# Kernel optimization log

Hardware: AMD Instinct MI355X
Metric: run time of the kernel (lower is better)

## Reference

```python
import jax, jax.numpy as jnp
import numpy as np

K = 4          # torus_dim (circles)
M = 6          # n_modes
GRID = 12      # grid_size for Laplacian eigenvalues
T = 2.0        # uniformity temperature
SPREAD_W = 1.0
B = 8192       # batch size


def _karmonic_weights():
    # lambda_n = 2 - 2 cos(2 pi n / N), n = 1..M; w = (lam - lam1)/(lam_max - lam1)
    n = np.arange(1, M + 1)
    lam = 2.0 - 2.0 * np.cos(2.0 * np.pi * n / GRID)
    w = (lam - lam[0]) / (lam.max() - lam[0])
    return jnp.asarray(w, dtype=jnp.float32)


def setup_inputs() -> dict:
    key = jax.random.key(0)
    k1, k2 = jax.random.split(key)
    angles = jax.random.normal(k1, (B, K), dtype=jnp.float32)
    fourier_embed = jax.random.normal(k2, (B, 2 * K * M), dtype=jnp.float32)
    return {"angles": angles, "fourier_embed": fourier_embed}


def reference(angles, fourier_embed):
    Bn = fourier_embed.shape[0]
    w = _karmonic_weights()
    # group by mode: (B, M, 2K)
    x = fourier_embed.reshape(Bn, M, 2 * K)
    eye = jnp.eye(Bn, dtype=bool)
    log_Bm1 = jnp.log(jnp.float32(Bn - 1))

    total_unif = jnp.float32(0.0)
    mode_unifs = []
    for n in range(M):  # fixed small structural loop over modes
        xn = x[:, n, :]                                   # (B, 2K)
        sq = jnp.sum(xn * xn, axis=1)                     # (B,)
        d2 = sq[:, None] + sq[None, :] - 2.0 * (xn @ xn.T)
        d2 = jnp.maximum(d2, 0.0)                         # cdist(...)**2, clamped >= 0
        neg = jnp.where(eye, -jnp.inf, -T * d2)           # exclude diagonal like masked_select
        unif_n = jnp.mean(jax.nn.logsumexp(neg, axis=1)) - log_Bm1
        mode_unifs.append(unif_n)
        total_unif = total_unif + w[n] * unif_n

    # circular decorrelation (spread) across circle pairs, vectorized over pairs
    mu = jnp.arctan2(jnp.mean(jnp.sin(angles), axis=0),
                     jnp.mean(jnp.cos(angles), axis=0))   # (K,) circular means
    s = jnp.sin(angles - mu[None, :])                     # (B, K)
    cov = (s.T @ s) / jnp.float32(Bn)                     # (K, K) = mean(s_i * s_j)
    var = jnp.diagonal(cov)                               # mean(s_i^2)
    den = jnp.sqrt(var[:, None] * var[None, :] + 1e-8)
    corr2 = (cov / den) ** 2
    iu = np.triu_indices(K, 1)                            # upper-triangle pairs i<j
    spread = jnp.mean(corr2[iu])

    total = total_unif + jnp.float32(SPREAD_W) * spread
    return total_unif, spread, total, jnp.stack(mode_unifs)
```

## Files before the change

kernel.cpp:

```cpp
#include <hip/hip_runtime.h>
#include <math.h>

constexpr int BN = 8192;
constexpr int MN = 6;

constexpr float TL    = 2.8853900817779268f;
constexpr float SCL_Z = 2.4022448795936154f;

typedef __bf16 bf16_t;
typedef bf16_t bf16x8 __attribute__((ext_vector_type(8)));
typedef float f32x4 __attribute__((ext_vector_type(4)));

union PK { bf16_t h[8]; uint4 u; };

__device__ __forceinline__ bf16x8 frag_of(uint4 u) {
    return __builtin_bit_cast(bf16x8, u);
}

__device__ __host__ __forceinline__ int midx(int a, int b) {
    return 8 * a - (a * (a - 1)) / 2 + (b - a);
}


__global__ __launch_bounds__(256) void prep_ang(const float* __restrict__ x,
                                                const float* __restrict__ ang,
                                                uint4* __restrict__ C,
                                                float* __restrict__ angp) {
    const int blk = blockIdx.x;
    const int tid = threadIdx.x;
    if (blk < 192) {
        int idx = blk * 256 + tid;
        int n = idx >> 13;
        int j = idx & (BN - 1);
        const float* p = x + (size_t)j * 48 + n * 8;

        PK zh, zl, a3, b3;
        float sq = 0.f;
#pragma unroll
        for (int k = 0; k < 8; ++k) {
            float v = p[k];
            sq = fmaf(v, v, sq);
            float z = SCL_Z * v;
            bf16_t h = (bf16_t)z;
            zh.h[k] = h;
            zl.h[k] = (bf16_t)(z - (float)h);
        }
        float s = -TL * sq;
        bf16_t sh = (bf16_t)s;
        bf16_t sl = (bf16_t)(s - (float)sh);
        bf16_t one = (bf16_t)1.0f, zero = (bf16_t)0.0f;
        a3.h[0] = one; a3.h[1] = one; a3.h[2] = sh;  a3.h[3] = sl;
        b3.h[0] = sh;  b3.h[1] = sl;  b3.h[2] = one; b3.h[3] = one;
#pragma unroll
        for (int k = 4; k < 8; ++k) { a3.h[k] = zero; b3.h[k] = zero; }

        size_t base = ((size_t)(n * 512 + (j >> 4))) * 64 + (j & 15);
        C[base +  0] = zh.u;
        C[base + 16] = zl.u;
        C[base + 32] = a3.u;
        C[base + 48] = b3.u;
    } else {
        const int i = (blk - 192) * 256 + tid;
        float v[8];
#pragma unroll
        for (int k = 0; k < 4; ++k) __sincosf(ang[i * 4 + k], &v[k], &v[4 + k]);
        float acc[44];
        int c = 0;
#pragma unroll
        for (int a = 0; a < 8; ++a)
#pragma unroll
            for (int bq = a; bq < 8; ++bq) acc[c++] = v[a] * v[bq];
#pragma unroll
        for (int a = 0; a < 8; ++a) acc[36 + a] = v[a];

#pragma unroll
        for (int q = 0; q < 44; ++q) {
            float s = acc[q];
            s += __shfl_xor(s, 1);  s += __shfl_xor(s, 2);
            s += __shfl_xor(s, 4);  s += __shfl_xor(s, 8);
            s += __shfl_xor(s, 16); s += __shfl_xor(s, 32);
            acc[q] = s;
        }
        __shared__ float sm[4][44];
        const int w = tid >> 6, lane = tid & 63;
        if (lane == 0)
#pragma unroll
            for (int q = 0; q < 44; ++q) sm[w][q] = acc[q];
        __syncthreads();
        if (tid < 44)
            angp[(blk - 192) * 44 + tid] =
                sm[0][tid] + sm[1][tid] + sm[2][tid] + sm[3][tid];
    }
}

__global__ __launch_bounds__(512, 6) void pair_sweep(const uint4* __restrict__ C,
                                                     float* __restrict__ colsumP,
                                                     unsigned short* __restrict__ credP) {
    const int tid  = threadIdx.x;
    const int lane = tid & 63;
    const int w    = __builtin_amdgcn_readfirstlane(tid >> 6);
    const int b    = blockIdx.x;
    const int m    = b >> 7;
    const int sp   = (b >> 1) & 63;
    const int h    = b & 1;
    const int rho  = 2 * w + h;

    __shared__ float cred[8192];
    __shared__ float smem[8][64];
    for (int q = tid; q < 8192; q += 512) cred[q] = 0.f;
    __syncthreads();

    const int g  = lane >> 4;
    const int pa = (g == 3) ? 2 : (g & 1);
    const int pb = (g == 3) ? 3 : (g >> 1);
    const int cl = lane & 15;
    const f32x4 z4 = {0.f, 0.f, 0.f, 0.f};
    const uint4* mbase = C + (size_t)m * 512 * 64;
    const uint4* bcol  = mbase + pb * 16 + cl;

#pragma unroll 1
    for (int sidx = 0; sidx < 2; ++sidx) {
        const int s = sidx ? (127 - sp) : sp;

        bf16x8 af[4];
#pragma unroll
        for (int t = 0; t < 4; ++t)
            af[t] = frag_of(mbase[(size_t)(4 * s + t) * 64 + pa * 16 + cl]);

        float racc[16];
#pragma unroll
        for (int q = 0; q < 16; ++q) racc[q] = 0.f;

        const int start = 4 * s + 4;
        const int first = start + (int)(((unsigned)(rho - start)) & 15u);
        const int f0 = (first < 512) ? first : 0;

        uint4 b0 = bcol[(size_t)f0 * 64];
        uint4 b1 = bcol[(size_t)(f0 + 16) * 64];
        for (int jt = first; jt < 512; jt += 16) {
            uint4 p0 = bcol[(size_t)(jt + 32) * 64];
            bf16x8 bf = frag_of(b0);
            float rsum = 0.f;
#pragma unroll
            for (int t = 0; t < 4; ++t) {
                f32x4 d = __builtin_amdgcn_mfma_f32_16x16x32_bf16(af[t], bf, z4, 0, 0, 0);
#pragma unroll
                for (int r = 0; r < 4; ++r) {
                    float e = __builtin_amdgcn_exp2f(d[r]);
                    racc[t * 4 + r] += e;
                    rsum += e;
                }
            }
            rsum += __shfl_xor(rsum, 16);
            rsum += __shfl_xor(rsum, 32);
            if (lane < 16) cred[jt * 16 + lane] += rsum;
            b0 = b1; b1 = p0;
        }

#pragma unroll
        for (int q = 0; q < 16; ++q) {
            float v = racc[q];
            v += __shfl_xor(v, 1);
            v += __shfl_xor(v, 2);
            v += __shfl_xor(v, 4);
            v += __shfl_xor(v, 8);
            racc[q] = v;
        }
        if (cl == 0) {
#pragma unroll
            for (int t = 0; t < 4; ++t)
#pragma unroll
                for (int r = 0; r < 4; ++r)
                    smem[w][t * 16 + g * 4 + r] = racc[t * 4 + r];
        }
        __syncthreads();
        if (tid < 64) {
            float ssum = 0.f;
#pragma unroll
            for (int ww = 0; ww < 8; ++ww) ssum += smem[ww][tid];
            colsumP[(size_t)h * (MN * BN) + m * BN + s * 64 + tid] = ssum;
        }
        __syncthreads();
    }

    for (int q = tid; q < 4096; q += 512) {
        int jt = 2 * (q >> 4) + h, c = q & 15;
        bf16_t v = (bf16_t)cred[jt * 16 + c];
        credP[((size_t)((m * 64 + sp) * 2 + h)) * 4096 + q] =
            __builtin_bit_cast(unsigned short, v);
    }
}

__global__ __launch_bounds__(256) void wedge(const uint4* __restrict__ C,
                                             float* __restrict__ wedgeP) {
    const int tid  = threadIdx.x;
    const int lane = tid & 63;
    const int wl   = tid >> 6;
    const int gw   = blockIdx.x * 4 + wl;
    const int m    = gw >> 7;
    const int s    = gw & 127;

    const int g  = lane >> 4;
    const int pa = (g == 3) ? 2 : (g & 1);
    const int pb = (g == 3) ? 3 : (g >> 1);
    const int cl = lane & 15;
    const int dd = cl - 4 * g;
    const f32x4 z4 = {0.f, 0.f, 0.f, 0.f};
    const uint4* mbase = C + (size_t)m * 512 * 64;

    bf16x8 af[4];
#pragma unroll
    for (int t = 0; t < 4; ++t)
        af[t] = frag_of(mbase[(size_t)(4 * s + t) * 64 + pa * 16 + cl]);

    float racc[16];
#pragma unroll
    for (int q = 0; q < 16; ++q) racc[q] = 0.f;

#pragma unroll
    for (int u = 0; u < 4; ++u) {
        bf16x8 bf = frag_of(mbase[(size_t)(4 * s + u) * 64 + pb * 16 + cl]);
#pragma unroll
        for (int t = 0; t < 4; ++t) {
            f32x4 d = __builtin_amdgcn_mfma_f32_16x16x32_bf16(af[t], bf, z4, 0, 0, 0);
#pragma unroll
            for (int r = 0; r < 4; ++r) {
                float e = __builtin_amdgcn_exp2f(d[r]);
                if (u == t) e = (dd == r) ? 0.f : e;
                racc[t * 4 + r] += e;
            }
        }
    }

#pragma unroll
    for (int q = 0; q < 16; ++q) {
        float v = racc[q];
        v += __shfl_xor(v, 1);
        v += __shfl_xor(v, 2);
        v += __shfl_xor(v, 4);
        v += __shfl_xor(v, 8);
        racc[q] = v;
    }

    __shared__ float smem[4][64];
    if (cl == 0) {
#pragma unroll
        for (int t = 0; t < 4; ++t)
#pragma unroll
            for (int r = 0; r < 4; ++r)
                smem[wl][t * 16 + g * 4 + r] = racc[t * 4 + r];
    }
    float val = smem[wl][lane];
    wedgeP[(size_t)m * BN + s * 64 + lane] = val;
}

__global__ __launch_bounds__(512) void log_red(const float* __restrict__ colsumP,
                                               const float* __restrict__ wedgeP,
                                               const unsigned short* __restrict__ credP,
                                               float* __restrict__ lp) {
    const int tid = threadIdx.x;
    const int idx = blockIdx.x * 512 + tid;
    const int m = idx >> 13;
    const int i = idx & (BN - 1);
    const int jt = i >> 4, c = i & 15;
    const int hh = jt & 1;
    const int q = (jt >> 1) * 16 + c;

    float v = wedgeP[idx] + colsumP[idx] + colsumP[MN * BN + idx];
    const unsigned short* base = credP + ((size_t)(m * 128 + hh)) * 4096 + q;
#pragma unroll 8
    for (int sp = 0; sp < 64; ++sp) {
        unsigned short u = base[(size_t)sp * 8192];
        v += (float)__builtin_bit_cast(bf16_t, u);
    }
    float lg = logf(v);
    lg += __shfl_xor(lg, 1);
    lg += __shfl_xor(lg, 2);
    lg += __shfl_xor(lg, 4);
    lg += __shfl_xor(lg, 8);
    lg += __shfl_xor(lg, 16);
    lg += __shfl_xor(lg, 32);
    __shared__ float sm[8];
    if ((tid & 63) == 0) sm[tid >> 6] = lg;
    __syncthreads();
    if (tid == 0) {
        float s = 0.f;
#pragma unroll
        for (int k = 0; k < 8; ++k) s += sm[k];
        lp[blockIdx.x] = s;
    }
}

__global__ __launch_bounds__(64) void final_asm(const float* __restrict__ angp,
                                                const float* __restrict__ lp,
                                                float* __restrict__ out) {
    const int tid = threadIdx.x;
    __shared__ float mom[44];

    if (tid < 44) {
        float s = 0.f;
        for (int bk = 0; bk < 32; ++bk) s += angp[bk * 44 + tid];
        mom[tid] = s;
    }
    __syncthreads();

    if (tid == 0) {
        float sm[4], cm[4];
#pragma unroll
        for (int k = 0; k < 4; ++k) {
            float S = mom[36 + k], Cc = mom[40 + k];
            float hyp = sqrtf(S * S + Cc * Cc);
            sm[k] = S / hyp;
            cm[k] = Cc / hyp;
        }
        auto COV = [&](int k, int l) -> float {
            int ks = k < l ? k : l, kl = k < l ? l : k;
            float mss = mom[midx(ks, kl)];
            float msc_kl = mom[midx(k, l + 4)];
            float msc_lk = mom[midx(l, k + 4)];
            float mcc = mom[midx(ks + 4, kl + 4)];
            return (cm[k] * cm[l] * mss - cm[k] * sm[l] * msc_kl -
                    sm[k] * cm[l] * msc_lk + sm[k] * sm[l] * mcc) *
                   (1.0f / (float)BN);
        };
        float var[4] = {COV(0, 0), COV(1, 1), COV(2, 2), COV(3, 3)};
        float spread = 0.f;
        const int pk[6] = {0, 0, 0, 1, 1, 2};
        const int pl[6] = {1, 2, 3, 2, 3, 3};
#pragma unroll
        for (int p = 0; p < 6; ++p) {
            float cv = COV(pk[p], pl[p]);
            float den = sqrtf(var[pk[p]] * var[pl[p]] + 1e-8f);
            float cr = cv / den;
            spread += cr * cr;
        }
        spread *= (1.0f / 6.0f);

        const float wgt[6] = {0.0f, 0.19615242270663188f, 0.4641016151377544f,
                              0.7320508075688773f, 0.9282032302755088f, 1.0f};
        const float logBm1 = logf((float)(BN - 1));
        float total_unif = 0.f, unif[6];
#pragma unroll
        for (int mm = 0; mm < 6; ++mm) {
            float s = 0.f;
            for (int k = 0; k < 16; ++k) s += lp[mm * 16 + k];
            unif[mm] = s * (1.0f / (float)BN) - logBm1;
            total_unif += wgt[mm] * unif[mm];
        }
        out[0] = total_unif;
        out[1] = spread;
        out[2] = total_unif + spread;
#pragma unroll
        for (int mm = 0; mm < 6; ++mm) out[3 + mm] = unif[mm];
    }
}

extern "C" void kernel_launch(void* const* d_in, const int* in_sizes, int n_in,
                              void* d_out, int out_size, void* d_ws, size_t ws_size,
                              hipStream_t stream) {
    const float* angles  = (const float*)d_in[0];
    const float* fourier = (const float*)d_in[1];
    float* out = (float*)d_out;

    char* ws = (char*)d_ws;
    uint4* C              = (uint4*)(ws + 0);
    unsigned short* credP = (unsigned short*)(ws + 3145728);
    float* colsumP        = (float*)(ws + 9437184);
    float* wedgeP         = (float*)(ws + 9830400);
    float* lp             = (float*)(ws + 10027008);
    float* angp           = (float*)(ws + 10027392);

    prep_ang<<<dim3(224), dim3(256), 0, stream>>>(fourier, angles, C, angp);
    pair_sweep<<<dim3(768), dim3(512), 0, stream>>>(C, colsumP, credP);
    wedge<<<dim3(192), dim3(256), 0, stream>>>(C, wedgeP);
    log_red<<<dim3(96), dim3(512), 0, stream>>>(colsumP, wedgeP, credP, lp);
    final_asm<<<dim3(1), dim3(64), 0, stream>>>(angp, lp, out);
}
```

Measured before the change: 61.36 us.

## Fuse wedge kernel into pair sweep, unroll tile loop by two, halve LDS

Removes the separate wedge kernel launch by having one wave per block (chosen per sweep half) compute the diagonal-tile contribution inside pair_sweep and add it to its row accumulators. The tile loop is unrolled by two with doubled prefetch so more MFMA and exp2 work is independent. The LDS column buffer is compacted to only the tiles matching this block's parity, and the colsum reduction is deferred to a single barrier at the end. This adds load imbalance on the wave doing the wedge and more register pressure under the 6-block occupancy bound.

```diff
diff --git a/kernel.cpp b/kernel.cpp
--- a/kernel.cpp
+++ b/kernel.cpp
@@ -105,9 +105,9 @@
     const int h    = b & 1;
     const int rho  = 2 * w + h;
 
-    __shared__ float cred[8192];
-    __shared__ float smem[8][64];
-    for (int q = tid; q < 8192; q += 512) cred[q] = 0.f;
+    __shared__ float cred[4096];
+    __shared__ float smem[2][8][64];
+    for (int q = tid; q < 4096; q += 512) cred[q] = 0.f;
     __syncthreads();
 
     const int g  = lane >> 4;
@@ -133,28 +133,89 @@
 
         const int start = 4 * s + 4;
         const int first = start + (int)(((unsigned)(rho - start)) & 15u);
-        const int f0 = (first < 512) ? first : 0;
-
-        uint4 b0 = bcol[(size_t)f0 * 64];
-        uint4 b1 = bcol[(size_t)(f0 + 16) * 64];
-        for (int jt = first; jt < 512; jt += 16) {
+        int jt  = first;
+        int cnt = (first < 512) ? (((512 - first) + 15) >> 4) : 0;
+
+        uint4 b0 = bcol[(size_t)((cnt > 0) ? jt : 0) * 64];
+        uint4 b1 = bcol[(size_t)((cnt > 1) ? (jt + 16) : 0) * 64];
+        while (cnt >= 2) {
             uint4 p0 = bcol[(size_t)(jt + 32) * 64];
-            bf16x8 bf = frag_of(b0);
-            float rsum = 0.f;
+            uint4 p1 = bcol[(size_t)(jt + 48) * 64];
+
+            bf16x8 bfA = frag_of(b0);
+            bf16x8 bfB = frag_of(b1);
+            float etA[4], etB[4];
 #pragma unroll
             for (int t = 0; t < 4; ++t) {
-                f32x4 d = __builtin_amdgcn_mfma_f32_16x16x32_bf16(af[t], bf, z4, 0, 0, 0);
-#pragma unroll
-                for (int r = 0; r < 4; ++r) {
-                    float e = __builtin_amdgcn_exp2f(d[r]);
-                    racc[t * 4 + r] += e;
-                    rsum += e;
+                f32x4 dA = __builtin_amdgcn_mfma_f32_16x16x32_bf16(af[t], bfA, z4, 0, 0, 0);
+                f32x4 dB = __builtin_amdgcn_mfma_f32_16x16x32_bf16(af[t], bfB, z4, 0, 0, 0);
+                float eA0 = __builtin_amdgcn_exp2f(dA[0]);
+                float eA1 = __builtin_amdgcn_exp2f(dA[1]);
+                float eA2 = __builtin_amdgcn_exp2f(dA[2]);
+                float eA3 = __builtin_amdgcn_exp2f(dA[3]);
+                float eB0 = __builtin_amdgcn_exp2f(dB[0]);
+                float eB1 = __builtin_amdgcn_exp2f(dB[1]);
+                float eB2 = __builtin_amdgcn_exp2f(dB[2]);
+                float eB3 = __builtin_amdgcn_exp2f(dB[3]);
+                racc[t * 4 + 0] += eA0; racc[t * 4 + 0] += eB0;
+                racc[t * 4 + 1] += eA1; racc[t * 4 + 1] += eB1;
+                racc[t * 4 + 2] += eA2; racc[t * 4 + 2] += eB2;
+                racc[t * 4 + 3] += eA3; racc[t * 4 + 3] += eB3;
+                etA[t] = (eA0 + eA1) + (eA2 + eA3);
+                etB[t] = (eB0 + eB1) + (eB2 + eB3);
+            }
+            float rA = (etA[0] + etA[1]) + (etA[2] + etA[3]);
+            float rB = (etB[0] + etB[1]) + (etB[2] + etB[3]);
+            rA += __shfl_xor(rA, 16);
+            rA += __shfl_xor(rA, 32);
+            rB += __shfl_xor(rB, 16);
+            rB += __shfl_xor(rB, 32);
+            if (lane < 16) {
+                int cb = (jt >> 1) * 16 + lane;
+                cred[cb] += rA;
+                cred[cb + 128] += rB;
+            }
+            b0 = p0; b1 = p1;
+            jt += 32; cnt -= 2;
+        }
+        if (cnt == 1) {
+            bf16x8 bfA = frag_of(b0);
+            float etA[4];
+#pragma unroll
+            for (int t = 0; t < 4; ++t) {
+                f32x4 dA = __builtin_amdgcn_mfma_f32_16x16x32_bf16(af[t], bfA, z4, 0, 0, 0);
+                float e0 = __builtin_amdgcn_exp2f(dA[0]);
+                float e1 = __builtin_amdgcn_exp2f(dA[1]);
+                float e2 = __builtin_amdgcn_exp2f(dA[2]);
+                float e3 = __builtin_amdgcn_exp2f(dA[3]);
+                racc[t * 4 + 0] += e0;
+                racc[t * 4 + 1] += e1;
+                racc[t * 4 + 2] += e2;
+                racc[t * 4 + 3] += e3;
+                etA[t] = (e0 + e1) + (e2 + e3);
+            }
+            float rA = (etA[0] + etA[1]) + (etA[2] + etA[3]);
+            rA += __shfl_xor(rA, 16);
+            rA += __shfl_xor(rA, 32);
+            if (lane < 16) cred[(jt >> 1) * 16 + lane] += rA;
+        }
+
+        if (w == 7 - sidx) {
+            const int dd = cl - 4 * g;
+#pragma unroll
+            for (int u = 0; u < 4; ++u) {
+                bf16x8 bf = frag_of(mbase[(size_t)(4 * s + u) * 64 + pb * 16 + cl]);
+#pragma unroll
+                for (int t = 0; t < 4; ++t) {
+                    f32x4 d = __builtin_amdgcn_mfma_f32_16x16x32_bf16(af[t], bf, z4, 0, 0, 0);
+#pragma unroll
+                    for (int r = 0; r < 4; ++r) {
+                        float e = __builtin_amdgcn_exp2f(d[r]);
+                        if (u == t && dd == r) e = 0.f;
+                        racc[t * 4 + r] += e;
+                    }
                 }
             }
-            rsum += __shfl_xor(rsum, 16);
-            rsum += __shfl_xor(rsum, 32);
-            if (lane < 16) cred[jt * 16 + lane] += rsum;
-            b0 = b1; b1 = p0;
         }
 
 #pragma unroll
@@ -171,91 +232,29 @@
             for (int t = 0; t < 4; ++t)
 #pragma unroll
                 for (int r = 0; r < 4; ++r)
-                    smem[w][t * 16 + g * 4 + r] = racc[t * 4 + r];
-        }
-        __syncthreads();
-        if (tid < 64) {
-            float ssum = 0.f;
-#pragma unroll
-            for (int ww = 0; ww < 8; ++ww) ssum += smem[ww][tid];
-            colsumP[(size_t)h * (MN * BN) + m * BN + s * 64 + tid] = ssum;
-        }
-        __syncthreads();
+                    smem[sidx][w][t * 16 + g * 4 + r] = racc[t * 4 + r];
+        }
+    }
+
+    __syncthreads();
+
+    if (tid < 128) {
+        const int si = tid >> 6, row = tid & 63;
+        float ssum = 0.f;
+#pragma unroll
+        for (int ww = 0; ww < 8; ++ww) ssum += smem[si][ww][row];
+        const int s = si ? (127 - sp) : sp;
+        colsumP[(size_t)h * (MN * BN) + m * BN + s * 64 + row] = ssum;
     }
 
     for (int q = tid; q < 4096; q += 512) {
-        int jt = 2 * (q >> 4) + h, c = q & 15;
-        bf16_t v = (bf16_t)cred[jt * 16 + c];
+        bf16_t v = (bf16_t)cred[q];
         credP[((size_t)((m * 64 + sp) * 2 + h)) * 4096 + q] =
             __builtin_bit_cast(unsigned short, v);
     }
 }
 
-__global__ __launch_bounds__(256) void wedge(const uint4* __restrict__ C,
-                                             float* __restrict__ wedgeP) {
-    const int tid  = threadIdx.x;
-    const int lane = tid & 63;
-    const int wl   = tid >> 6;
-    const int gw   = blockIdx.x * 4 + wl;
-    const int m    = gw >> 7;
-    const int s    = gw & 127;
-
-    const int g  = lane >> 4;
-    const int pa = (g == 3) ? 2 : (g & 1);
-    const int pb = (g == 3) ? 3 : (g >> 1);
-    const int cl = lane & 15;
-    const int dd = cl - 4 * g;
-    const f32x4 z4 = {0.f, 0.f, 0.f, 0.f};
-    const uint4* mbase = C + (size_t)m * 512 * 64;
-
-    bf16x8 af[4];
-#pragma unroll
-    for (int t = 0; t < 4; ++t)
-        af[t] = frag_of(mbase[(size_t)(4 * s + t) * 64 + pa * 16 + cl]);
-
-    float racc[16];
-#pragma unroll
-    for (int q = 0; q < 16; ++q) racc[q] = 0.f;
-
-#pragma unroll
-    for (int u = 0; u < 4; ++u) {
-        bf16x8 bf = frag_of(mbase[(size_t)(4 * s + u) * 64 + pb * 16 + cl]);
-#pragma unroll
-        for (int t = 0; t < 4; ++t) {
-            f32x4 d = __builtin_amdgcn_mfma_f32_16x16x32_bf16(af[t], bf, z4, 0, 0, 0);
-#pragma unroll
-            for (int r = 0; r < 4; ++r) {
-                float e = __builtin_amdgcn_exp2f(d[r]);
-                if (u == t) e = (dd == r) ? 0.f : e;
-                racc[t * 4 + r] += e;
-            }
-        }
-    }
-
-#pragma unroll
-    for (int q = 0; q < 16; ++q) {
-        float v = racc[q];
-        v += __shfl_xor(v, 1);
-        v += __shfl_xor(v, 2);
-        v += __shfl_xor(v, 4);
-        v += __shfl_xor(v, 8);
-        racc[q] = v;
-    }
-
-    __shared__ float smem[4][64];
-    if (cl == 0) {
-#pragma unroll
-        for (int t = 0; t < 4; ++t)
-#pragma unroll
-            for (int r = 0; r < 4; ++r)
-                smem[wl][t * 16 + g * 4 + r] = racc[t * 4 + r];
-    }
-    float val = smem[wl][lane];
-    wedgeP[(size_t)m * BN + s * 64 + lane] = val;
-}
-
 __global__ __launch_bounds__(512) void log_red(const float* __restrict__ colsumP,
-                                               const float* __restrict__ wedgeP,
                                                const unsigned short* __restrict__ credP,
                                                float* __restrict__ lp) {
     const int tid = threadIdx.x;
@@ -266,7 +265,7 @@
     const int hh = jt & 1;
     const int q = (jt >> 1) * 16 + c;
 
-    float v = wedgeP[idx] + colsumP[idx] + colsumP[MN * BN + idx];
+    float v = colsumP[idx] + colsumP[MN * BN + idx];
     const unsigned short* base = credP + ((size_t)(m * 128 + hh)) * 4096 + q;
 #pragma unroll 8
     for (int sp = 0; sp < 64; ++sp) {
@@ -366,13 +365,11 @@
     uint4* C              = (uint4*)(ws + 0);
     unsigned short* credP = (unsigned short*)(ws + 3145728);
     float* colsumP        = (float*)(ws + 9437184);
-    float* wedgeP         = (float*)(ws + 9830400);
-    float* lp             = (float*)(ws + 10027008);
-    float* angp           = (float*)(ws + 10027392);
+    float* lp             = (float*)(ws + 9830400);
+    float* angp           = (float*)(ws + 9830784);
 
     prep_ang<<<dim3(224), dim3(256), 0, stream>>>(fourier, angles, C, angp);
     pair_sweep<<<dim3(768), dim3(512), 0, stream>>>(C, colsumP, credP);
-    wedge<<<dim3(192), dim3(256), 0, stream>>>(C, wedgeP);
-    log_red<<<dim3(96), dim3(512), 0, stream>>>(colsumP, wedgeP, credP, lp);
+    log_red<<<dim3(96), dim3(512), 0, stream>>>(colsumP, credP, lp);
     final_asm<<<dim3(1), dim3(64), 0, stream>>>(angp, lp, out);
 }
```

After: 66.25 us. 1.08x slower.

## Fold diagonal wedge tiles into pair_sweep and coalesce credP layout

Applied to the files above, without the earlier changes.

Removes the separate wedge kernel by having one idle-ish wave per sidx iteration in pair_sweep compute the diagonal block tile with masked self-terms. The per-sidx column-sum reduction now goes through a double-buffered shared array, which drops two block barriers per iteration in favour of one at the end. credP is re-laid out so log_red reads it contiguously by idx. The trade is extra load imbalance on waves 6 and 7 inside pair_sweep, in exchange for one fewer launch, no wedgeP round trip, and coalesced reads in the reduction.

```diff
diff --git a/kernel.cpp b/kernel.cpp
--- a/kernel.cpp
+++ b/kernel.cpp
@@ -106,7 +106,7 @@
     const int rho  = 2 * w + h;
 
     __shared__ float cred[8192];
-    __shared__ float smem[8][64];
+    __shared__ float smem[2][8][64];
     for (int q = tid; q < 8192; q += 512) cred[q] = 0.f;
     __syncthreads();
 
@@ -157,6 +157,24 @@
             b0 = b1; b1 = p0;
         }
 
+        if (w == 7 - sidx) {
+            const int dd = cl - 4 * g;
+#pragma unroll
+            for (int u = 0; u < 4; ++u) {
+                bf16x8 bf = frag_of(mbase[(size_t)(4 * s + u) * 64 + pb * 16 + cl]);
+#pragma unroll
+                for (int t = 0; t < 4; ++t) {
+                    f32x4 d = __builtin_amdgcn_mfma_f32_16x16x32_bf16(af[t], bf, z4, 0, 0, 0);
+#pragma unroll
+                    for (int r = 0; r < 4; ++r) {
+                        float e = __builtin_amdgcn_exp2f(d[r]);
+                        if (u == t && dd == r) e = 0.f;
+                        racc[t * 4 + r] += e;
+                    }
+                }
+            }
+        }
+
 #pragma unroll
         for (int q = 0; q < 16; ++q) {
             float v = racc[q];
@@ -171,106 +189,39 @@
             for (int t = 0; t < 4; ++t)
 #pragma unroll
                 for (int r = 0; r < 4; ++r)
-                    smem[w][t * 16 + g * 4 + r] = racc[t * 4 + r];
-        }
-        __syncthreads();
-        if (tid < 64) {
-            float ssum = 0.f;
-#pragma unroll
-            for (int ww = 0; ww < 8; ++ww) ssum += smem[ww][tid];
-            colsumP[(size_t)h * (MN * BN) + m * BN + s * 64 + tid] = ssum;
-        }
-        __syncthreads();
+                    smem[sidx][w][t * 16 + g * 4 + r] = racc[t * 4 + r];
+        }
+    }
+
+    __syncthreads();
+
+    if (tid < 128) {
+        const int si = tid >> 6, row = tid & 63;
+        float ssum = 0.f;
+#pragma unroll
+        for (int ww = 0; ww < 8; ++ww) ssum += smem[si][ww][row];
+        const int s = si ? (127 - sp) : sp;
+        colsumP[(size_t)h * (MN * BN) + m * BN + s * 64 + row] = ssum;
     }
 
     for (int q = tid; q < 4096; q += 512) {
-        int jt = 2 * (q >> 4) + h, c = q & 15;
+        const int jt = 2 * (q >> 4) + h, c = q & 15;
         bf16_t v = (bf16_t)cred[jt * 16 + c];
-        credP[((size_t)((m * 64 + sp) * 2 + h)) * 4096 + q] =
+        credP[(size_t)sp * (MN * BN) + m * BN + jt * 16 + c] =
             __builtin_bit_cast(unsigned short, v);
     }
 }
 
-__global__ __launch_bounds__(256) void wedge(const uint4* __restrict__ C,
-                                             float* __restrict__ wedgeP) {
-    const int tid  = threadIdx.x;
-    const int lane = tid & 63;
-    const int wl   = tid >> 6;
-    const int gw   = blockIdx.x * 4 + wl;
-    const int m    = gw >> 7;
-    const int s    = gw & 127;
-
-    const int g  = lane >> 4;
-    const int pa = (g == 3) ? 2 : (g & 1);
-    const int pb = (g == 3) ? 3 : (g >> 1);
-    const int cl = lane & 15;
-    const int dd = cl - 4 * g;
-    const f32x4 z4 = {0.f, 0.f, 0.f, 0.f};
-    const uint4* mbase = C + (size_t)m * 512 * 64;
-
-    bf16x8 af[4];
-#pragma unroll
-    for (int t = 0; t < 4; ++t)
-        af[t] = frag_of(mbase[(size_t)(4 * s + t) * 64 + pa * 16 + cl]);
-
-    float racc[16];
-#pragma unroll
-    for (int q = 0; q < 16; ++q) racc[q] = 0.f;
-
-#pragma unroll
-    for (int u = 0; u < 4; ++u) {
-        bf16x8 bf = frag_of(mbase[(size_t)(4 * s + u) * 64 + pb * 16 + cl]);
-#pragma unroll
-        for (int t = 0; t < 4; ++t) {
-            f32x4 d = __builtin_amdgcn_mfma_f32_16x16x32_bf16(af[t], bf, z4, 0, 0, 0);
-#pragma unroll
-            for (int r = 0; r < 4; ++r) {
-                float e = __builtin_amdgcn_exp2f(d[r]);
-                if (u == t) e = (dd == r) ? 0.f : e;
-                racc[t * 4 + r] += e;
-            }
-        }
-    }
-
-#pragma unroll
-    for (int q = 0; q < 16; ++q) {
-        float v = racc[q];
-        v += __shfl_xor(v, 1);
-        v += __shfl_xor(v, 2);
-        v += __shfl_xor(v, 4);
-        v += __shfl_xor(v, 8);
-        racc[q] = v;
-    }
-
-    __shared__ float smem[4][64];
-    if (cl == 0) {
-#pragma unroll
-        for (int t = 0; t < 4; ++t)
-#pragma unroll
-            for (int r = 0; r < 4; ++r)
-                smem[wl][t * 16 + g * 4 + r] = racc[t * 4 + r];
-    }
-    float val = smem[wl][lane];
-    wedgeP[(size_t)m * BN + s * 64 + lane] = val;
-}
-
 __global__ __launch_bounds__(512) void log_red(const float* __restrict__ colsumP,
-                                               const float* __restrict__ wedgeP,
                                                const unsigned short* __restrict__ credP,
                                                float* __restrict__ lp) {
     const int tid = threadIdx.x;
     const int idx = blockIdx.x * 512 + tid;
-    const int m = idx >> 13;
-    const int i = idx & (BN - 1);
-    const int jt = i >> 4, c = i & 15;
-    const int hh = jt & 1;
-    const int q = (jt >> 1) * 16 + c;
-
-    float v = wedgeP[idx] + colsumP[idx] + colsumP[MN * BN + idx];
-    const unsigned short* base = credP + ((size_t)(m * 128 + hh)) * 4096 + q;
+
+    float v = colsumP[idx] + colsumP[MN * BN + idx];
 #pragma unroll 8
     for (int sp = 0; sp < 64; ++sp) {
-        unsigned short u = base[(size_t)sp * 8192];
+        unsigned short u = credP[(size_t)sp * (MN * BN) + idx];
         v += (float)__builtin_bit_cast(bf16_t, u);
     }
     float lg = logf(v);
@@ -366,13 +317,11 @@
     uint4* C              = (uint4*)(ws + 0);
     unsigned short* credP = (unsigned short*)(ws + 3145728);
     float* colsumP        = (float*)(ws + 9437184);
-    float* wedgeP         = (float*)(ws + 9830400);
-    float* lp             = (float*)(ws + 10027008);
-    float* angp           = (float*)(ws + 10027392);
+    float* lp             = (float*)(ws + 9830400);
+    float* angp           = (float*)(ws + 9830784);
 
     prep_ang<<<dim3(224), dim3(256), 0, stream>>>(fourier, angles, C, angp);
     pair_sweep<<<dim3(768), dim3(512), 0, stream>>>(C, colsumP, credP);
-    wedge<<<dim3(192), dim3(256), 0, stream>>>(C, wedgeP);
-    log_red<<<dim3(96), dim3(512), 0, stream>>>(colsumP, wedgeP, credP, lp);
+    log_red<<<dim3(96), dim3(512), 0, stream>>>(colsumP, credP, lp);
     final_asm<<<dim3(1), dim3(64), 0, stream>>>(angp, lp, out);
 }
```

After: 62.31 us. Within noise of the previous version (+1.5%).
